# Kernel optimization log

Measured on AMD Instinct MI355X. Metric: run time of the kernel, lower is better.

Reference implementation:

```python
import jax, jax.numpy as jnp
import numpy as np
from jax import lax

G0, G1 = 16, 16
UNITS = 256


def setup_inputs() -> dict:
    key = jax.random.key(0)
    ks = jax.random.split(key, 20)
    B, H, W, C = 64, 512, 512, 3
    U = UNITS
    flat = 12 * 12 * 3  # after two VALID 3x3 convs on 16x16x3
    inp = {
        'image': jax.random.normal(ks[0], (B, H, W, C), jnp.float32),
        'section': jax.random.uniform(ks[1], (B, 3), jnp.float32),
        'h0': jax.random.normal(ks[2], (B, U), jnp.float32) * 0.1,
        'c0': jax.random.normal(ks[3], (B, U), jnp.float32) * 0.1,
        'conv1_k': jax.random.normal(ks[4], (3, 3, C, 3), jnp.float32) * 0.2,
        'conv1_b': jnp.zeros((3,), jnp.float32),
        'conv2_k': jax.random.normal(ks[5], (3, 3, 3, 3), jnp.float32) * 0.2,
        'conv2_b': jnp.zeros((3,), jnp.float32),
        'dense_w': jax.random.normal(ks[6], (flat, U), jnp.float32) * (1.0 / np.sqrt(flat)),
        'dense_b': jnp.zeros((U,), jnp.float32),
        'lstm_k': jax.random.normal(ks[7], (U, 4 * U), jnp.float32) * (1.0 / np.sqrt(U)),
        'lstm_rk': jax.random.normal(ks[8], (U, 4 * U), jnp.float32) * (1.0 / np.sqrt(U)),
        'lstm_b': jnp.zeros((4 * U,), jnp.float32),
        'nsc_w1': jax.random.normal(ks[9], (U, U), jnp.float32) * (1.0 / np.sqrt(U)),
        'nsc_b1': jnp.zeros((U,), jnp.float32),
        'nsc_w2': jax.random.normal(ks[10], (U, 3), jnp.float32) * (1.0 / np.sqrt(U)),
        'nsc_b2': jnp.zeros((3,), jnp.float32),
    }
    return inp


def _interpolate(image, section):
    # image: (B,H,W,C); section: (B,3) = (x, y, scale); coords in [0,1],
    # mapped linearly onto grid indices with constant (clamp) extension,
    # matching tfp.math.batch_interp_regular_nd_grid over image axes 1,2.
    B, H, W, C = image.shape
    starts = section[:, :2]                       # (B,2)
    stops = section[:, :2] + section[:, 2:]       # (B,2) broadcast scale
    t0 = jnp.linspace(0.0, 1.0, G0)               # along grid_dim[0]
    alpha = jnp.linspace(0.0, 1.0, G1)            # along grid_dim[1]
    # p0[b,i,j]: coordinate mapped to image axis 1 (H)
    p0 = (starts[:, 0, None] + t0[None, :] * (stops[:, 0] - starts[:, 0])[:, None])[:, :, None]
    p0 = jnp.broadcast_to(p0, (B, G0, G1))
    # p1[b,i,j]: coordinate mapped to image axis 2 (W)
    p1 = (starts[:, 1, None] + alpha[None, :] * (stops[:, 1] - starts[:, 1])[:, None])[:, None, :]
    p1 = jnp.broadcast_to(p1, (B, G0, G1))
    fy = jnp.clip(p0 * (H - 1), 0.0, H - 1)
    fx = jnp.clip(p1 * (W - 1), 0.0, W - 1)
    y0 = jnp.floor(fy).astype(jnp.int32)
    x0 = jnp.floor(fx).astype(jnp.int32)
    y1 = jnp.minimum(y0 + 1, H - 1)
    x1 = jnp.minimum(x0 + 1, W - 1)
    wy = (fy - y0)[..., None]
    wx = (fx - x0)[..., None]
    b = jnp.arange(B)[:, None, None]
    v00 = image[b, y0, x0]
    v01 = image[b, y0, x1]
    v10 = image[b, y1, x0]
    v11 = image[b, y1, x1]
    top = v00 * (1 - wx) + v01 * wx
    bot = v10 * (1 - wx) + v11 * wx
    return top * (1 - wy) + bot * wy            # (B,G0,G1,C)


def _conv_relu(x, k, b):
    y = lax.conv_general_dilated(x, k, (1, 1), 'VALID',
                                 dimension_numbers=('NHWC', 'HWIO', 'NHWC'))
    return jax.nn.relu(y + b)


def reference(image, section, h0, c0, conv1_k, conv1_b, conv2_k, conv2_b,
              dense_w, dense_b, lstm_k, lstm_rk, lstm_b,
              nsc_w1, nsc_b1, nsc_w2, nsc_b2):
    sec = _interpolate(image, section)                 # (B,16,16,C)
    x = _conv_relu(sec, conv1_k, conv1_b)              # (B,14,14,3)
    x = _conv_relu(x, conv2_k, conv2_b)                # (B,12,12,3)
    x = x.reshape(x.shape[0], -1)                      # (B,432)
    x = jax.nn.relu(x @ dense_w + dense_b)             # (B,U)
    # Keras LSTMCell: gate order i, f, g(c), o
    z = x @ lstm_k + h0 @ lstm_rk + lstm_b
    i, f, g, o = jnp.split(z, 4, axis=-1)
    c_new = jax.nn.sigmoid(f) * c0 + jax.nn.sigmoid(i) * jnp.tanh(g)
    h_new = jax.nn.sigmoid(o) * jnp.tanh(c_new)
    nsc = jax.nn.relu(h_new @ nsc_w1 + nsc_b1)
    next_section = jax.nn.sigmoid(nsc @ nsc_w2 + nsc_b2)  # (B,3)
    return h_new, c_new, next_section
```

## Files before the change

### kernel.cpp

```cpp
#include <hip/hip_runtime.h>
#include <math.h>

#define BATCH 64
#define IMH 512
#define IMW 512
#define UNITS 256

__device__ __forceinline__ float sigmoidf_(float x) {
    return 1.0f / (1.0f + __expf(-x));
}
__device__ __forceinline__ float tanhf_(float x) {
    float e = __expf(2.0f * x);
    return 1.0f - 2.0f / (e + 1.0f);
}

__global__ __launch_bounds__(1024) void fused_cell_kernel(
    const float* __restrict__ image,
    const float* __restrict__ section,
    const float* __restrict__ h0,
    const float* __restrict__ c0,
    const float* __restrict__ k1,
    const float* __restrict__ b1,
    const float* __restrict__ k2,
    const float* __restrict__ b2,
    const float* __restrict__ dw,
    const float* __restrict__ db,
    const float* __restrict__ lk,
    const float* __restrict__ lrk,
    const float* __restrict__ lb,
    const float* __restrict__ w1,
    const float* __restrict__ nb1,
    const float* __restrict__ w2,
    const float* __restrict__ nb2,
    float* __restrict__ out)
{
    const int b   = blockIdx.x;
    const int tid = threadIdx.x;

    __shared__ float s_sec[16][16][3];
    __shared__ float s_c1[14][14][3];
    __shared__ float s_flat[432];
    __shared__ float s_x[256];
    __shared__ float s_h0[256];
    __shared__ float s_hn[256];
    __shared__ float s_nsc[256];
    __shared__ float s_z[1024];
    __shared__ float s_part[4][256];
    __shared__ float s_k1[84];
    __shared__ float s_k2[84];

    if (tid < 81)       s_k1[tid]      = k1[tid];
    else if (tid < 84)  s_k1[tid]      = b1[tid - 81];
    else if (tid < 165) s_k2[tid - 84] = k2[tid - 84];
    else if (tid < 168) s_k2[tid - 84] = b2[tid - 165];
    if (tid < 256) s_h0[tid] = h0[b * UNITS + tid];

    if (tid < 256) {
        const float s0 = section[b * 3 + 0];
        const float s1 = section[b * 3 + 1];
        const float s2 = section[b * 3 + 2];
        const int i = tid >> 4, j = tid & 15;
        float p0 = s0 + (float)i * (1.0f / 15.0f) * s2;
        float p1 = s1 + (float)j * (1.0f / 15.0f) * s2;
        float fy = fminf(fmaxf(p0 * 511.0f, 0.0f), 511.0f);
        float fx = fminf(fmaxf(p1 * 511.0f, 0.0f), 511.0f);
        int y0 = (int)floorf(fy);
        int x0 = (int)floorf(fx);
        int y1 = min(y0 + 1, 511);
        int x1 = min(x0 + 1, 511);
        float wy = fy - (float)y0;
        float wx = fx - (float)x0;
        const float* base = image + (size_t)b * IMH * IMW * 3;
        const float* p00 = base + (y0 * IMW + x0) * 3;
        const float* p01 = base + (y0 * IMW + x1) * 3;
        const float* p10 = base + (y1 * IMW + x0) * 3;
        const float* p11 = base + (y1 * IMW + x1) * 3;
        #pragma unroll
        for (int c = 0; c < 3; ++c) {
            float top = p00[c] * (1.0f - wx) + p01[c] * wx;
            float bot = p10[c] * (1.0f - wx) + p11[c] * wx;
            s_sec[i][j][c] = top * (1.0f - wy) + bot * wy;
        }
    }
    __syncthreads();

    if (tid < 196) {
        const int i = tid / 14, j = tid % 14;
        float a0 = s_k1[81], a1 = s_k1[82], a2 = s_k1[83];
        #pragma unroll
        for (int di = 0; di < 3; ++di)
            #pragma unroll
            for (int dj = 0; dj < 3; ++dj)
                #pragma unroll
                for (int ci = 0; ci < 3; ++ci) {
                    float v = s_sec[i + di][j + dj][ci];
                    const int kb = ((di * 3 + dj) * 3 + ci) * 3;
                    a0 += v * s_k1[kb + 0];
                    a1 += v * s_k1[kb + 1];
                    a2 += v * s_k1[kb + 2];
                }
        s_c1[i][j][0] = fmaxf(a0, 0.0f);
        s_c1[i][j][1] = fmaxf(a1, 0.0f);
        s_c1[i][j][2] = fmaxf(a2, 0.0f);
    }
    __syncthreads();

    if (tid < 144) {
        const int i = tid / 12, j = tid % 12;
        float a0 = s_k2[81], a1 = s_k2[82], a2 = s_k2[83];
        #pragma unroll
        for (int di = 0; di < 3; ++di)
            #pragma unroll
            for (int dj = 0; dj < 3; ++dj)
                #pragma unroll
                for (int ci = 0; ci < 3; ++ci) {
                    float v = s_c1[i + di][j + dj][ci];
                    const int kb = ((di * 3 + dj) * 3 + ci) * 3;
                    a0 += v * s_k2[kb + 0];
                    a1 += v * s_k2[kb + 1];
                    a2 += v * s_k2[kb + 2];
                }
        const int fb = tid * 3;
        s_flat[fb + 0] = fmaxf(a0, 0.0f);
        s_flat[fb + 1] = fmaxf(a1, 0.0f);
        s_flat[fb + 2] = fmaxf(a2, 0.0f);
    }
    __syncthreads();

    {
        const int g = tid >> 8, col = tid & 255;
        const float* wp = dw + (g * 108) * 256 + col;
        const float* fp = s_flat + g * 108;
        float acc = 0.0f;
        #pragma unroll 6
        for (int k = 0; k < 108; ++k)
            acc += fp[k] * wp[k * 256];
        s_part[g][col] = acc;
    }
    __syncthreads();
    if (tid < 256)
        s_x[tid] = fmaxf(s_part[0][tid] + s_part[1][tid] + s_part[2][tid] +
                         s_part[3][tid] + db[tid], 0.0f);
    __syncthreads();

    {
        float z = lb[tid];
        const float* lkp = lk  + tid;
        const float* lrp = lrk + tid;
        #pragma unroll 8
        for (int k = 0; k < 256; ++k)
            z += s_x[k] * lkp[k * 1024] + s_h0[k] * lrp[k * 1024];
        s_z[tid] = z;
    }
    __syncthreads();
    if (tid < 256) {
        const float zi = s_z[tid];
        const float zf = s_z[256 + tid];
        const float zg = s_z[512 + tid];
        const float zo = s_z[768 + tid];
        const float cprev = c0[b * UNITS + tid];
        const float cn = sigmoidf_(zf) * cprev + sigmoidf_(zi) * tanhf_(zg);
        const float hn = sigmoidf_(zo) * tanhf_(cn);
        out[b * UNITS + tid] = hn;
        out[BATCH * UNITS + b * UNITS + tid] = cn;
        s_hn[tid] = hn;
    }
    __syncthreads();

    {
        const int g = tid >> 8, col = tid & 255;
        const float* wp = w1 + (g * 64) * 256 + col;
        const float* hp = s_hn + g * 64;
        float acc = 0.0f;
        #pragma unroll 8
        for (int k = 0; k < 64; ++k)
            acc += hp[k] * wp[k * 256];
        s_part[g][col] = acc;
    }
    __syncthreads();
    if (tid < 256)
        s_nsc[tid] = fmaxf(s_part[0][tid] + s_part[1][tid] + s_part[2][tid] +
                           s_part[3][tid] + nb1[tid], 0.0f);
    __syncthreads();

    if (tid < 192) {
        const int j = tid >> 6;
        const int l = tid & 63;
        float p = 0.0f;
        #pragma unroll
        for (int k = l; k < 256; k += 64)
            p += s_nsc[k] * w2[k * 3 + j];
        #pragma unroll
        for (int off = 32; off > 0; off >>= 1)
            p += __shfl_down(p, off);
        if (l == 0)
            out[2 * BATCH * UNITS + b * 3 + j] = sigmoidf_(p + nb2[j]);
    }
}

extern "C" void kernel_launch(void* const* d_in, const int* in_sizes, int n_in,
                              void* d_out, int out_size, void* d_ws, size_t ws_size,
                              hipStream_t stream) {
    const float* image   = (const float*)d_in[0];
    const float* section = (const float*)d_in[1];
    const float* h0      = (const float*)d_in[2];
    const float* c0      = (const float*)d_in[3];
    const float* k1      = (const float*)d_in[4];
    const float* b1      = (const float*)d_in[5];
    const float* k2      = (const float*)d_in[6];
    const float* b2      = (const float*)d_in[7];
    const float* dw      = (const float*)d_in[8];
    const float* db      = (const float*)d_in[9];
    const float* lk      = (const float*)d_in[10];
    const float* lrk     = (const float*)d_in[11];
    const float* lb      = (const float*)d_in[12];
    const float* w1      = (const float*)d_in[13];
    const float* nb1     = (const float*)d_in[14];
    const float* w2      = (const float*)d_in[15];
    const float* nb2     = (const float*)d_in[16];
    float* out = (float*)d_out;

    fused_cell_kernel<<<BATCH, 1024, 0, stream>>>(
        image, section, h0, c0, k1, b1, k2, b2, dw, db,
        lk, lrk, lb, w1, nb1, w2, nb2, out);
}
```

Measured before the change: 299.5 us.

## Split fused cell into prep, batched LSTM GEMM, and NSC kernels

Replaces the single per-batch-row kernel with three kernels. The prep kernel runs interpolation, convs and the dense layer over four blocks per batch row and writes x, h0 and c0 transposed to the workspace. The LSTM kernel gives each block two hidden columns across all 64 batch rows, so each LSTM weight is read once rather than 64 times, and the NSC head runs as its own kernel. This cuts the redundant weight traffic and raises parallelism, but adds two launches, workspace round trips and 128KB of shared memory per LSTM block.

```diff
diff --git a/kernel.cpp b/kernel.cpp
--- a/kernel.cpp
+++ b/kernel.cpp
@@ -6,6 +6,10 @@
 #define IMW 512
 #define UNITS 256
 
+#define WS_XT   0
+#define WS_H0T  16384
+#define WS_C0T  32768
+
 __device__ __forceinline__ float sigmoidf_(float x) {
     return 1.0f / (1.0f + __expf(-x));
 }
@@ -14,7 +18,7 @@
     return 1.0f - 2.0f / (e + 1.0f);
 }
 
-__global__ __launch_bounds__(1024) void fused_cell_kernel(
+__global__ __launch_bounds__(256) void prep_kernel(
     const float* __restrict__ image,
     const float* __restrict__ section,
     const float* __restrict__ h0,
@@ -25,27 +29,16 @@
     const float* __restrict__ b2,
     const float* __restrict__ dw,
     const float* __restrict__ db,
-    const float* __restrict__ lk,
-    const float* __restrict__ lrk,
-    const float* __restrict__ lb,
-    const float* __restrict__ w1,
-    const float* __restrict__ nb1,
-    const float* __restrict__ w2,
-    const float* __restrict__ nb2,
-    float* __restrict__ out)
+    float* __restrict__ ws)
 {
-    const int b   = blockIdx.x;
+    const int b   = blockIdx.x >> 2;
+    const int q   = blockIdx.x & 3;
     const int tid = threadIdx.x;
 
     __shared__ float s_sec[16][16][3];
     __shared__ float s_c1[14][14][3];
     __shared__ float s_flat[432];
-    __shared__ float s_x[256];
-    __shared__ float s_h0[256];
-    __shared__ float s_hn[256];
-    __shared__ float s_nsc[256];
-    __shared__ float s_z[1024];
-    __shared__ float s_part[4][256];
+    __shared__ float s_part[4][64];
     __shared__ float s_k1[84];
     __shared__ float s_k2[84];
 
@@ -53,9 +46,8 @@
     else if (tid < 84)  s_k1[tid]      = b1[tid - 81];
     else if (tid < 165) s_k2[tid - 84] = k2[tid - 84];
     else if (tid < 168) s_k2[tid - 84] = b2[tid - 165];
-    if (tid < 256) s_h0[tid] = h0[b * UNITS + tid];
-
-    if (tid < 256) {
+
+    {
         const float s0 = section[b * 3 + 0];
         const float s1 = section[b * 3 + 1];
         const float s2 = section[b * 3 + 2];
@@ -128,43 +120,104 @@
     __syncthreads();
 
     {
-        const int g = tid >> 8, col = tid & 255;
-        const float* wp = dw + (g * 108) * 256 + col;
-        const float* fp = s_flat + g * 108;
+        const int l = tid & 63, kg = tid >> 6;
+        const int col = q * 64 + l;
+        const float* wp = dw + (kg * 108) * 256 + col;
+        const float* fp = s_flat + kg * 108;
         float acc = 0.0f;
         #pragma unroll 6
         for (int k = 0; k < 108; ++k)
             acc += fp[k] * wp[k * 256];
-        s_part[g][col] = acc;
-    }
-    __syncthreads();
-    if (tid < 256)
-        s_x[tid] = fmaxf(s_part[0][tid] + s_part[1][tid] + s_part[2][tid] +
-                         s_part[3][tid] + db[tid], 0.0f);
-    __syncthreads();
-
-    {
-        float z = lb[tid];
-        const float* lkp = lk  + tid;
-        const float* lrp = lrk + tid;
+        s_part[kg][l] = acc;
+    }
+    __syncthreads();
+    if (tid < 64) {
+        const int col = q * 64 + tid;
+        float x = fmaxf(s_part[0][tid] + s_part[1][tid] + s_part[2][tid] +
+                        s_part[3][tid] + db[col], 0.0f);
+        ws[WS_XT + col * 64 + b] = x;
+    }
+    if (q == 0) {
+        ws[WS_H0T + tid * 64 + b] = h0[b * 256 + tid];
+        ws[WS_C0T + tid * 64 + b] = c0[b * 256 + tid];
+    }
+}
+
+__global__ __launch_bounds__(512) void lstm_kernel(
+    const float* __restrict__ lk,
+    const float* __restrict__ lrk,
+    const float* __restrict__ lb,
+    const float* __restrict__ ws,
+    float* __restrict__ out)
+{
+    const int j   = blockIdx.x;
+    const int tid = threadIdx.x;
+
+    __shared__ float s_x[256][64];
+    __shared__ float s_h[256][64];
+    __shared__ float s_z[8][65];
+
+    {
+        const float4* srcx = (const float4*)(ws + WS_XT);
+        const float4* srch = (const float4*)(ws + WS_H0T);
+        float4* dstx = (float4*)&s_x[0][0];
+        float4* dsth = (float4*)&s_h[0][0];
+        #pragma unroll
+        for (int idx = tid; idx < 4096; idx += 512) {
+            dstx[idx] = srcx[idx];
+            dsth[idx] = srch[idx];
+        }
+    }
+    __syncthreads();
+
+    {
+        const int b  = tid & 63;
+        const int zc = tid >> 6;
+        const int g  = zc >> 1;
+        const int cl = zc & 1;
+        const int col  = j * 2 + cl;
+        const int zcol = g * 256 + col;
+        const float* lkp = lk  + zcol;
+        const float* lrp = lrk + zcol;
+        float acc = lb[zcol];
         #pragma unroll 8
         for (int k = 0; k < 256; ++k)
-            z += s_x[k] * lkp[k * 1024] + s_h0[k] * lrp[k * 1024];
-        s_z[tid] = z;
-    }
-    __syncthreads();
-    if (tid < 256) {
-        const float zi = s_z[tid];
-        const float zf = s_z[256 + tid];
-        const float zg = s_z[512 + tid];
-        const float zo = s_z[768 + tid];
-        const float cprev = c0[b * UNITS + tid];
+            acc += s_x[k][b] * lkp[k * 1024] + s_h[k][b] * lrp[k * 1024];
+        s_z[zc][b] = acc;
+    }
+    __syncthreads();
+
+    if (tid < 128) {
+        const int b  = tid >> 1;
+        const int cl = tid & 1;
+        const int col = j * 2 + cl;
+        const float zi = s_z[0 + cl][b];
+        const float zf = s_z[2 + cl][b];
+        const float zg = s_z[4 + cl][b];
+        const float zo = s_z[6 + cl][b];
+        const float cprev = ws[WS_C0T + col * 64 + b];
         const float cn = sigmoidf_(zf) * cprev + sigmoidf_(zi) * tanhf_(zg);
         const float hn = sigmoidf_(zo) * tanhf_(cn);
-        out[b * UNITS + tid] = hn;
-        out[BATCH * UNITS + b * UNITS + tid] = cn;
-        s_hn[tid] = hn;
-    }
+        out[b * UNITS + col] = hn;
+        out[BATCH * UNITS + b * UNITS + col] = cn;
+    }
+}
+
+__global__ __launch_bounds__(1024) void nsc_kernel(
+    const float* __restrict__ w1,
+    const float* __restrict__ nb1,
+    const float* __restrict__ w2,
+    const float* __restrict__ nb2,
+    float* __restrict__ out)
+{
+    const int b   = blockIdx.x;
+    const int tid = threadIdx.x;
+
+    __shared__ float s_hn[256];
+    __shared__ float s_nsc[256];
+    __shared__ float s_part[4][256];
+
+    if (tid < 256) s_hn[tid] = out[b * UNITS + tid];
     __syncthreads();
 
     {
@@ -219,8 +272,10 @@
     const float* w2      = (const float*)d_in[15];
     const float* nb2     = (const float*)d_in[16];
     float* out = (float*)d_out;
-
-    fused_cell_kernel<<<BATCH, 1024, 0, stream>>>(
-        image, section, h0, c0, k1, b1, k2, b2, dw, db,
-        lk, lrk, lb, w1, nb1, w2, nb2, out);
-}
+    float* ws  = (float*)d_ws;
+
+    prep_kernel<<<256, 256, 0, stream>>>(
+        image, section, h0, c0, k1, b1, k2, b2, dw, db, ws);
+    lstm_kernel<<<128, 512, 0, stream>>>(lk, lrk, lb, ws, out);
+    nsc_kernel<<<64, 1024, 0, stream>>>(w1, nb1, w2, nb2, out);
+}
```

Result: no change. 299.6 us (+0.0%).
